# Performance work log

Measured on AMD Instinct MI355X. Metric: run time of the kernel, lower is better.

The kernel has to match this reference:

```python
import jax, jax.numpy as jnp
import numpy as np

NUM_HEADS = 8


def setup_inputs() -> dict:
    B, S, D, Q, SEG = 4, 4096, 512, 1, 256
    key = jax.random.key(0)
    ks = jax.random.split(key, 7)
    x = jax.random.normal(ks[0], (B, S, D), dtype=jnp.float32)
    seg_id = jnp.sort(jax.random.randint(ks[1], (B, S), 0, SEG), axis=-1)
    # ensure every row actually spans segment ids 0..SEG-1 so max()+1 == SEG
    seg_id = seg_id.at[:, 0].set(0).at[:, -1].set(SEG - 1)
    valid_mask = jnp.ones((B, S), dtype=bool)
    query_bank = jax.random.normal(ks[2], (1, 1, Q, D), dtype=jnp.float32)
    scale = 0.02
    w_q = jax.random.normal(ks[3], (D, D), dtype=jnp.float32) * scale
    w_k = jax.random.normal(ks[4], (D, D), dtype=jnp.float32) * scale
    w_v = jax.random.normal(ks[5], (D, D), dtype=jnp.float32) * scale
    w_o = jax.random.normal(ks[6], (D, D), dtype=jnp.float32) * scale
    return {"x": x, "seg_id": seg_id, "valid_mask": valid_mask, "s_seg_max": SEG,
            "query_bank": query_bank, "w_q": w_q, "w_k": w_k, "w_v": w_v, "w_o": w_o}


def reference(x, seg_id, valid_mask, s_seg_max, query_bank, w_q, w_k, w_v, w_o):
    B, S, D = x.shape
    Q = query_bank.shape[2]
    H = NUM_HEADS
    hd = D // H
    L = s_seg_max * Q  # number of pooled queries

    # expand learned query bank over batch and segments, project (Linear: x @ W.T)
    queries = jnp.broadcast_to(query_bank, (B, s_seg_max, Q, D)).reshape(B, L, D)
    q = (queries @ w_q.T).reshape(B, L, H, hd).transpose(0, 2, 1, 3)   # bhqd
    k = (x @ w_k.T).reshape(B, S, H, hd).transpose(0, 2, 1, 3)         # bhkd
    v = (x @ w_v.T).reshape(B, S, H, hd).transpose(0, 2, 1, 3)         # bhkd

    # torch SDPA boolean mask semantics: True = participate in attention
    seg_for_query = jnp.repeat(jnp.arange(s_seg_max), Q)               # [L]
    attend = (seg_id[:, None, :] != seg_for_query[None, :, None]) | (~valid_mask[:, None, :])  # [B,L,S]

    scores = jnp.einsum('bhqd,bhkd->bhqk', q, k) / np.sqrt(hd).astype(x.dtype)
    scores = jnp.where(attend[:, None, :, :], scores, -jnp.inf)
    attn = jax.nn.softmax(scores, axis=-1)
    out = jnp.einsum('bhqk,bhkd->bhqd', attn, v)                       # [B,H,L,hd]
    out = out.transpose(0, 2, 1, 3).reshape(B, L, D)
    return out @ w_o.T
```

## Files before the change

kernel.cpp:

```cpp
#include <hip/hip_runtime.h>
#include <hip/hip_bf16.h>


#define S 4096
#define D 512
#define H 8
#define SEG 256
#define NROW 1024

typedef short bf16x8 __attribute__((ext_vector_type(8)));
typedef float fvec4  __attribute__((ext_vector_type(4)));

constexpr int OFF_SEGO   = 0;
constexpr int OFF_DSEG   = 1032;
constexpr int OFF_NALL   = 9224;
constexpr int OFF_C16    = 11272;
constexpr int OFF_PSEG_F = 15368;
constexpr int OFF_NSEG_F = 2112520;
constexpr size_t WS_FLOATS = 2374664;

static __device__ inline ushort f2bf(float f) {
    __hip_bfloat16 h = __float2bfloat16(f);
    return *reinterpret_cast<ushort*>(&h);
}
static __device__ inline float bf2f(ushort u) {
    return __uint_as_float(((uint)u) << 16);
}
static __device__ inline uint pack2(float a, float b) {
    return (uint)f2bf(a) | ((uint)f2bf(b) << 16);
}

__global__ __launch_bounds__(512) void k_setup(const float* __restrict__ qb,
        const float* __restrict__ w_q, const float* __restrict__ w_k,
        const int* __restrict__ seg_id, float* __restrict__ W) {
    int tid = threadIdx.x, blk = blockIdx.x;
    if (blk < 8) {
        __shared__ float qbs[D];
        __shared__ float part[64][9];
        __shared__ float qp[64];
        int h = blk;
        qbs[tid] = qb[tid];
        __syncthreads();
        int jj = tid >> 3, p = tid & 7;
        const float* wr = w_q + (size_t)(h*64 + jj)*D;
        float a = 0.f;
        for (int t = 0; t < 64; ++t) a += qbs[p + 8*t] * wr[p + 8*t];
        part[jj][p] = a;
        __syncthreads();
        if (tid < 64) {
            float s = 0.f;
            #pragma unroll
            for (int p2 = 0; p2 < 8; ++p2) s += part[tid][p2];
            qp[tid] = s;
        }
        __syncthreads();
        float c = 0.f;
        for (int j2 = 0; j2 < 64; ++j2)
            c += qp[j2] * w_k[(size_t)(h*64 + j2)*D + tid];
        ((ushort*)(W + OFF_C16))[h*512 + tid] = f2bf(c * 0.125f);
    } else if (blk < 12) {
        int b = blk - 8;
        if (tid <= SEG) {
            const int* sid = seg_id + (size_t)b*S;
            int lo = 0, hi = S;
            while (lo < hi) { int mid = (lo+hi) >> 1; if (sid[mid] < tid) lo = mid+1; else hi = mid; }
            ((int*)(W + OFF_SEGO))[b*(SEG+1) + tid] = lo;
        }
    } else {
        for (int t = tid; t < 4*D; t += 512) W[OFF_NALL + t] = 0.f;
        uint* c16u = (uint*)(W + OFF_C16);
        #pragma unroll
        for (int j = 0; j < 4; ++j) c16u[2048 + tid*4 + j] = 0u;
    }
}

__global__ __launch_bounds__(256) void k_pseg(const float* __restrict__ x,
                                              float* __restrict__ W) {
    __shared__ ushort xs[32][520];
    __shared__ ushort cls[16][520];
    __shared__ float E_lds[32][12];
    int row = blockIdx.x, b = row >> 8, l = row & 255, tid = threadIdx.x;
    const ushort* c16g = (const ushort*)(W + OFF_C16);
    #pragma unroll
    for (int rep = 0; rep < 4; ++rep) {
        int q = rep*256 + tid, r = q >> 6, c8 = q & 63;
        *(bf16x8*)&cls[r][c8*8] = *(const bf16x8*)&c16g[r*512 + c8*8];
    }
    const int* off = (const int*)(W + OFF_SEGO);
    int k0 = off[b*(SEG+1) + l], k1 = off[b*(SEG+1) + l + 1];
    float2 acc[8]; float es[8];
    #pragma unroll
    for (int h = 0; h < 8; ++h) { acc[h] = make_float2(0.f,0.f); es[h] = 0.f; }
    int lane = tid & 63, wave = tid >> 6;

    for (int kc = k0; kc < k1; kc += 32) {
        int nk = min(32, k1 - kc);
        __syncthreads();
        #pragma unroll
        for (int rep = 0; rep < 16; ++rep) {
            int t4 = rep*256 + tid, r = t4 >> 7, c4 = t4 & 127;
            if (r < nk) {
                float4 v = ((const float4*)(x + (size_t)(b*S + kc + r)*D))[c4];
                uint2 u; u.x = pack2(v.x, v.y); u.y = pack2(v.z, v.w);
                *(uint2*)&xs[r][c4*4] = u;
            }
        }
        __syncthreads();
        if (wave < 2 && wave*16 < nk) {
            int m = lane & 15, kg = lane >> 4;
            fvec4 sc = {0,0,0,0};
            for (int ks = 0; ks < 512; ks += 32) {
                bf16x8 a  = *(const bf16x8*)&xs[wave*16 + m][ks + kg*8];
                bf16x8 bb = *(const bf16x8*)&cls[m][ks + kg*8];
                sc = __builtin_amdgcn_mfma_f32_16x16x32_bf16(a, bb, sc, 0, 0, 0);
            }
            int h = m;
            #pragma unroll
            for (int r = 0; r < 4; ++r) {
                int kl = wave*16 + kg*4 + r;
                if (h < 8 && kl < nk) E_lds[kl][h] = __expf(sc[r]);
            }
        }
        __syncthreads();
        for (int kk = 0; kk < nk; ++kk) {
            uint xv = *(const uint*)&xs[kk][2*tid];
            float x0 = bf2f((ushort)(xv & 0xffff));
            float x1 = bf2f((ushort)(xv >> 16));
            float4 ea = *(const float4*)&E_lds[kk][0];
            float4 eb = *(const float4*)&E_lds[kk][4];
            float e[8] = {ea.x,ea.y,ea.z,ea.w,eb.x,eb.y,eb.z,eb.w};
            #pragma unroll
            for (int h = 0; h < 8; ++h) {
                acc[h].x += e[h]*x0;
                acc[h].y += e[h]*x1;
                es[h]    += e[h];
            }
        }
    }
    uint* Pb = (uint*)(W + OFF_PSEG_F);
    #pragma unroll
    for (int h = 0; h < 8; ++h)
        Pb[(size_t)row*2048 + h*256 + tid] = pack2(acc[h].x, acc[h].y);
    if (tid == 0) {
        #pragma unroll
        for (int h = 0; h < 8; ++h) W[OFF_DSEG + row*8 + h] = es[h];
    }
}

__global__ __launch_bounds__(256) void k_gemm_v(const float* __restrict__ w_v,
                                                float* __restrict__ W) {
    __shared__ ushort As[32][520];
    __shared__ ushort Bs[64][520];
    __shared__ float colsum[2][64];
    int rt = blockIdx.x, h = blockIdx.y, tid = threadIdx.x;
    const ushort* Pb = (const ushort*)(W + OFF_PSEG_F);
    #pragma unroll
    for (int rep = 0; rep < 8; ++rep) {
        int idx = rep*256 + tid, r = idx >> 6, j = idx & 63;
        *(bf16x8*)&As[r][j*8] =
            *(const bf16x8*)&Pb[(size_t)((rt*32 + r)*8 + h)*512 + j*8];
    }
    #pragma unroll
    for (int rep = 0; rep < 32; ++rep) {
        int idx = rep*256 + tid, r = idx >> 7, c4 = idx & 127;
        float4 v = ((const float4*)(w_v + (size_t)(h*64 + r)*512))[c4];
        uint2 u; u.x = pack2(v.x, v.y); u.y = pack2(v.z, v.w);
        *(uint2*)&Bs[r][c4*4] = u;
    }
    __syncthreads();
    int lane = tid & 63, w = tid >> 6;
    int wm = w & 1, wn = w >> 1;
    int m = lane & 15, kg = lane >> 4;
    fvec4 acc0 = {0,0,0,0}, acc1 = {0,0,0,0};
    for (int ks = 0; ks < 512; ks += 32) {
        bf16x8 a  = *(const bf16x8*)&As[wm*16 + m][ks + kg*8];
        bf16x8 b0 = *(const bf16x8*)&Bs[wn*32 + m][ks + kg*8];
        bf16x8 b1 = *(const bf16x8*)&Bs[wn*32 + 16 + m][ks + kg*8];
        acc0 = __builtin_amdgcn_mfma_f32_16x16x32_bf16(a, b0, acc0, 0, 0, 0);
        acc1 = __builtin_amdgcn_mfma_f32_16x16x32_bf16(a, b1, acc1, 0, 0, 0);
    }
    ushort* NSb = (ushort*)(W + OFF_NSEG_F);
    int rowbase = rt*32 + wm*16 + kg*4;
    int col0 = h*64 + wn*32 + m, col1 = col0 + 16;
    float s0 = 0.f, s1 = 0.f;
    #pragma unroll
    for (int r = 0; r < 4; ++r) {
        NSb[(size_t)(rowbase + r)*512 + col0] = f2bf(acc0[r]);
        NSb[(size_t)(rowbase + r)*512 + col1] = f2bf(acc1[r]);
        s0 += acc0[r]; s1 += acc1[r];
    }
    s0 += __shfl_xor(s0, 16); s0 += __shfl_xor(s0, 32);
    s1 += __shfl_xor(s1, 16); s1 += __shfl_xor(s1, 32);
    if (lane < 16) {
        colsum[wm][wn*32 + lane]      = s0;
        colsum[wm][wn*32 + 16 + lane] = s1;
    }
    __syncthreads();
    if (tid < 64) {
        int b = rt >> 3;
        atomicAdd(&W[OFF_NALL + b*512 + h*64 + tid], colsum[0][tid] + colsum[1][tid]);
    }
}

__global__ __launch_bounds__(256) void k_gemm_o(const float* __restrict__ w_o,
                                                float* __restrict__ W,
                                                float* __restrict__ out) {
    __shared__ ushort As[32][520];
    __shared__ ushort Bs[64][520];
    __shared__ float NAl[512];
    __shared__ float dpart[8][8];
    __shared__ float invs[32][8];
    int rt = blockIdx.x, nt = blockIdx.y, tid = threadIdx.x;
    int b = rt >> 3;
    if (tid < 64) {
        int h = tid >> 3, sg = tid & 7;
        float s = 0.f;
        for (int l2 = sg*32; l2 < sg*32 + 32; ++l2)
            s += W[OFF_DSEG + (b*256 + l2)*8 + h];
        dpart[h][sg] = s;
    }
    NAl[tid]       = W[OFF_NALL + b*512 + tid];
    NAl[tid + 256] = W[OFF_NALL + b*512 + tid + 256];
    __syncthreads();
    {
        int r = tid >> 3, h = tid & 7;
        float da = 0.f;
        #pragma unroll
        for (int sg = 0; sg < 8; ++sg) da += dpart[h][sg];
        invs[r][h] = 1.f / (da - W[OFF_DSEG + (rt*32 + r)*8 + h]);
    }
    #pragma unroll
    for (int rep = 0; rep < 32; ++rep) {
        int idx = rep*256 + tid, r = idx >> 7, c4 = idx & 127;
        float4 v = ((const float4*)(w_o + (size_t)(nt*64 + r)*512))[c4];
        uint2 u; u.x = pack2(v.x, v.y); u.y = pack2(v.z, v.w);
        *(uint2*)&Bs[r][c4*4] = u;
    }
    __syncthreads();
    const ushort* NSb = (const ushort*)(W + OFF_NSEG_F);
    #pragma unroll
    for (int rep = 0; rep < 8; ++rep) {
        int idx = rep*256 + tid, r = idx >> 6, j = idx & 63;
        bf16x8 ns = *(const bf16x8*)&NSb[(size_t)(rt*32 + r)*512 + j*8];
        float inv = invs[r][j >> 3];
        ushort o[8];
        #pragma unroll
        for (int e = 0; e < 8; ++e)
            o[e] = f2bf((NAl[j*8 + e] - bf2f((ushort)ns[e])) * inv);
        uint4 u;
        u.x = o[0] | ((uint)o[1] << 16);
        u.y = o[2] | ((uint)o[3] << 16);
        u.z = o[4] | ((uint)o[5] << 16);
        u.w = o[6] | ((uint)o[7] << 16);
        *(uint4*)&As[r][j*8] = u;
    }
    __syncthreads();
    int lane = tid & 63, w = tid >> 6;
    int wm = w & 1, wn = w >> 1;
    int m = lane & 15, kg = lane >> 4;
    fvec4 acc0 = {0,0,0,0}, acc1 = {0,0,0,0};
    for (int ks = 0; ks < 512; ks += 32) {
        bf16x8 a  = *(const bf16x8*)&As[wm*16 + m][ks + kg*8];
        bf16x8 b0 = *(const bf16x8*)&Bs[wn*32 + m][ks + kg*8];
        bf16x8 b1 = *(const bf16x8*)&Bs[wn*32 + 16 + m][ks + kg*8];
        acc0 = __builtin_amdgcn_mfma_f32_16x16x32_bf16(a, b0, acc0, 0, 0, 0);
        acc1 = __builtin_amdgcn_mfma_f32_16x16x32_bf16(a, b1, acc1, 0, 0, 0);
    }
    int rowb = rt*32 + wm*16 + kg*4;
    int col0 = nt*64 + wn*32 + m, col1 = col0 + 16;
    #pragma unroll
    for (int r = 0; r < 4; ++r) {
        out[(size_t)(rowb + r)*512 + col0] = acc0[r];
        out[(size_t)(rowb + r)*512 + col1] = acc1[r];
    }
}

extern "C" void kernel_launch(void* const* d_in, const int* in_sizes, int n_in,
                              void* d_out, int out_size, void* d_ws, size_t ws_size,
                              hipStream_t stream) {
    const float* x   = (const float*)d_in[0];
    const int*   seg = (const int*)d_in[1];
    const float* qb  = (const float*)d_in[4];
    const float* w_q = (const float*)d_in[5];
    const float* w_k = (const float*)d_in[6];
    const float* w_v = (const float*)d_in[7];
    const float* w_o = (const float*)d_in[8];
    float* W   = (float*)d_ws;
    float* out = (float*)d_out;

    if (ws_size < WS_FLOATS * sizeof(float)) return;

    hipLaunchKernelGGL(k_setup,  dim3(13),    dim3(512), 0, stream, qb, w_q, w_k, seg, W);
    hipLaunchKernelGGL(k_pseg,   dim3(NROW),  dim3(256), 0, stream, x, W);
    hipLaunchKernelGGL(k_gemm_v, dim3(32, 8), dim3(256), 0, stream, w_v, W);
    hipLaunchKernelGGL(k_gemm_o, dim3(32, 8), dim3(256), 0, stream, w_o, W, out);
}
```

Measured before the change: 37.60 us.

## Fuse pseg, V-GEMM and O-GEMM into one launch with flag-based dataflow sync

Merges the three post-setup kernels into a single 1536-block launch. Downstream blocks spin on per-row flags and per-batch counters in workspace instead of waiting at kernel boundaries, so GEMM work can overlap with the tail of the segment-pooling phase and two launch gaps go away. The GEMM stages now stream K in 128-wide chunks through smaller shared tiles, which lowers LDS use per block. The spin-waits depend on producer blocks being scheduled before their consumers and have a timeout fallback, which risks reading stale data or burning cycles while polling.

```diff
diff --git a/kernel.cpp b/kernel.cpp
--- a/kernel.cpp
+++ b/kernel.cpp
@@ -6,7 +6,6 @@
 #define D 512
 #define H 8
 #define SEG 256
-#define NROW 1024
 
 typedef short bf16x8 __attribute__((ext_vector_type(8)));
 typedef float fvec4  __attribute__((ext_vector_type(4)));
@@ -17,7 +16,9 @@
 constexpr int OFF_C16    = 11272;
 constexpr int OFF_PSEG_F = 15368;
 constexpr int OFF_NSEG_F = 2112520;
-constexpr size_t WS_FLOATS = 2374664;
+constexpr int OFF_FLAGS  = 2374664;
+constexpr int OFF_VCNT   = 2375688;
+constexpr size_t WS_FLOATS = 2375696;
 
 static __device__ inline ushort f2bf(float f) {
     __hip_bfloat16 h = __float2bfloat16(f);
@@ -71,207 +72,250 @@
         uint* c16u = (uint*)(W + OFF_C16);
         #pragma unroll
         for (int j = 0; j < 4; ++j) c16u[2048 + tid*4 + j] = 0u;
+        uint* fl = (uint*)(W + OFF_FLAGS);
+        for (int t = tid; t < 1028; t += 512) fl[t] = 0u;
     }
 }
 
-__global__ __launch_bounds__(256) void k_pseg(const float* __restrict__ x,
-                                              float* __restrict__ W) {
-    __shared__ ushort xs[32][520];
-    __shared__ ushort cls[16][520];
-    __shared__ float E_lds[32][12];
-    int row = blockIdx.x, b = row >> 8, l = row & 255, tid = threadIdx.x;
-    const ushort* c16g = (const ushort*)(W + OFF_C16);
-    #pragma unroll
-    for (int rep = 0; rep < 4; ++rep) {
-        int q = rep*256 + tid, r = q >> 6, c8 = q & 63;
-        *(bf16x8*)&cls[r][c8*8] = *(const bf16x8*)&c16g[r*512 + c8*8];
-    }
-    const int* off = (const int*)(W + OFF_SEGO);
-    int k0 = off[b*(SEG+1) + l], k1 = off[b*(SEG+1) + l + 1];
-    float2 acc[8]; float es[8];
-    #pragma unroll
-    for (int h = 0; h < 8; ++h) { acc[h] = make_float2(0.f,0.f); es[h] = 0.f; }
+__global__ __launch_bounds__(256) void k_fused(const float* __restrict__ x,
+        const float* __restrict__ w_v, const float* __restrict__ w_o,
+        float* __restrict__ W, float* __restrict__ out) {
+    __shared__ __align__(16) char sm[51456];
+    int tid = threadIdx.x, blk = blockIdx.x;
     int lane = tid & 63, wave = tid >> 6;
-
-    for (int kc = k0; kc < k1; kc += 32) {
-        int nk = min(32, k1 - kc);
-        __syncthreads();
-        #pragma unroll
-        for (int rep = 0; rep < 16; ++rep) {
-            int t4 = rep*256 + tid, r = t4 >> 7, c4 = t4 & 127;
-            if (r < nk) {
-                float4 v = ((const float4*)(x + (size_t)(b*S + kc + r)*D))[c4];
-                uint2 u; u.x = pack2(v.x, v.y); u.y = pack2(v.z, v.w);
-                *(uint2*)&xs[r][c4*4] = u;
-            }
-        }
-        __syncthreads();
-        if (wave < 2 && wave*16 < nk) {
-            int m = lane & 15, kg = lane >> 4;
-            fvec4 sc = {0,0,0,0};
-            for (int ks = 0; ks < 512; ks += 32) {
-                bf16x8 a  = *(const bf16x8*)&xs[wave*16 + m][ks + kg*8];
-                bf16x8 bb = *(const bf16x8*)&cls[m][ks + kg*8];
-                sc = __builtin_amdgcn_mfma_f32_16x16x32_bf16(a, bb, sc, 0, 0, 0);
-            }
-            int h = m;
-            #pragma unroll
-            for (int r = 0; r < 4; ++r) {
-                int kl = wave*16 + kg*4 + r;
-                if (h < 8 && kl < nk) E_lds[kl][h] = __expf(sc[r]);
-            }
-        }
-        __syncthreads();
-        for (int kk = 0; kk < nk; ++kk) {
-            uint xv = *(const uint*)&xs[kk][2*tid];
-            float x0 = bf2f((ushort)(xv & 0xffff));
-            float x1 = bf2f((ushort)(xv >> 16));
-            float4 ea = *(const float4*)&E_lds[kk][0];
-            float4 eb = *(const float4*)&E_lds[kk][4];
-            float e[8] = {ea.x,ea.y,ea.z,ea.w,eb.x,eb.y,eb.z,eb.w};
-            #pragma unroll
-            for (int h = 0; h < 8; ++h) {
-                acc[h].x += e[h]*x0;
-                acc[h].y += e[h]*x1;
-                es[h]    += e[h];
-            }
-        }
-    }
-    uint* Pb = (uint*)(W + OFF_PSEG_F);
-    #pragma unroll
-    for (int h = 0; h < 8; ++h)
-        Pb[(size_t)row*2048 + h*256 + tid] = pack2(acc[h].x, acc[h].y);
-    if (tid == 0) {
-        #pragma unroll
-        for (int h = 0; h < 8; ++h) W[OFF_DSEG + row*8 + h] = es[h];
-    }
-}
-
-__global__ __launch_bounds__(256) void k_gemm_v(const float* __restrict__ w_v,
-                                                float* __restrict__ W) {
-    __shared__ ushort As[32][520];
-    __shared__ ushort Bs[64][520];
-    __shared__ float colsum[2][64];
-    int rt = blockIdx.x, h = blockIdx.y, tid = threadIdx.x;
-    const ushort* Pb = (const ushort*)(W + OFF_PSEG_F);
-    #pragma unroll
-    for (int rep = 0; rep < 8; ++rep) {
-        int idx = rep*256 + tid, r = idx >> 6, j = idx & 63;
-        *(bf16x8*)&As[r][j*8] =
-            *(const bf16x8*)&Pb[(size_t)((rt*32 + r)*8 + h)*512 + j*8];
-    }
-    #pragma unroll
-    for (int rep = 0; rep < 32; ++rep) {
-        int idx = rep*256 + tid, r = idx >> 7, c4 = idx & 127;
-        float4 v = ((const float4*)(w_v + (size_t)(h*64 + r)*512))[c4];
-        uint2 u; u.x = pack2(v.x, v.y); u.y = pack2(v.z, v.w);
-        *(uint2*)&Bs[r][c4*4] = u;
-    }
-    __syncthreads();
-    int lane = tid & 63, w = tid >> 6;
-    int wm = w & 1, wn = w >> 1;
-    int m = lane & 15, kg = lane >> 4;
-    fvec4 acc0 = {0,0,0,0}, acc1 = {0,0,0,0};
-    for (int ks = 0; ks < 512; ks += 32) {
-        bf16x8 a  = *(const bf16x8*)&As[wm*16 + m][ks + kg*8];
-        bf16x8 b0 = *(const bf16x8*)&Bs[wn*32 + m][ks + kg*8];
-        bf16x8 b1 = *(const bf16x8*)&Bs[wn*32 + 16 + m][ks + kg*8];
-        acc0 = __builtin_amdgcn_mfma_f32_16x16x32_bf16(a, b0, acc0, 0, 0, 0);
-        acc1 = __builtin_amdgcn_mfma_f32_16x16x32_bf16(a, b1, acc1, 0, 0, 0);
-    }
-    ushort* NSb = (ushort*)(W + OFF_NSEG_F);
-    int rowbase = rt*32 + wm*16 + kg*4;
-    int col0 = h*64 + wn*32 + m, col1 = col0 + 16;
-    float s0 = 0.f, s1 = 0.f;
-    #pragma unroll
-    for (int r = 0; r < 4; ++r) {
-        NSb[(size_t)(rowbase + r)*512 + col0] = f2bf(acc0[r]);
-        NSb[(size_t)(rowbase + r)*512 + col1] = f2bf(acc1[r]);
-        s0 += acc0[r]; s1 += acc1[r];
-    }
-    s0 += __shfl_xor(s0, 16); s0 += __shfl_xor(s0, 32);
-    s1 += __shfl_xor(s1, 16); s1 += __shfl_xor(s1, 32);
-    if (lane < 16) {
-        colsum[wm][wn*32 + lane]      = s0;
-        colsum[wm][wn*32 + 16 + lane] = s1;
-    }
-    __syncthreads();
-    if (tid < 64) {
-        int b = rt >> 3;
-        atomicAdd(&W[OFF_NALL + b*512 + h*64 + tid], colsum[0][tid] + colsum[1][tid]);
-    }
-}
-
-__global__ __launch_bounds__(256) void k_gemm_o(const float* __restrict__ w_o,
-                                                float* __restrict__ W,
-                                                float* __restrict__ out) {
-    __shared__ ushort As[32][520];
-    __shared__ ushort Bs[64][520];
-    __shared__ float NAl[512];
-    __shared__ float dpart[8][8];
-    __shared__ float invs[32][8];
-    int rt = blockIdx.x, nt = blockIdx.y, tid = threadIdx.x;
-    int b = rt >> 3;
-    if (tid < 64) {
-        int h = tid >> 3, sg = tid & 7;
-        float s = 0.f;
-        for (int l2 = sg*32; l2 < sg*32 + 32; ++l2)
-            s += W[OFF_DSEG + (b*256 + l2)*8 + h];
-        dpart[h][sg] = s;
-    }
-    NAl[tid]       = W[OFF_NALL + b*512 + tid];
-    NAl[tid + 256] = W[OFF_NALL + b*512 + tid + 256];
-    __syncthreads();
-    {
-        int r = tid >> 3, h = tid & 7;
-        float da = 0.f;
-        #pragma unroll
-        for (int sg = 0; sg < 8; ++sg) da += dpart[h][sg];
-        invs[r][h] = 1.f / (da - W[OFF_DSEG + (rt*32 + r)*8 + h]);
-    }
-    #pragma unroll
-    for (int rep = 0; rep < 32; ++rep) {
-        int idx = rep*256 + tid, r = idx >> 7, c4 = idx & 127;
-        float4 v = ((const float4*)(w_o + (size_t)(nt*64 + r)*512))[c4];
-        uint2 u; u.x = pack2(v.x, v.y); u.y = pack2(v.z, v.w);
-        *(uint2*)&Bs[r][c4*4] = u;
-    }
-    __syncthreads();
-    const ushort* NSb = (const ushort*)(W + OFF_NSEG_F);
-    #pragma unroll
-    for (int rep = 0; rep < 8; ++rep) {
-        int idx = rep*256 + tid, r = idx >> 6, j = idx & 63;
-        bf16x8 ns = *(const bf16x8*)&NSb[(size_t)(rt*32 + r)*512 + j*8];
-        float inv = invs[r][j >> 3];
-        ushort o[8];
-        #pragma unroll
-        for (int e = 0; e < 8; ++e)
-            o[e] = f2bf((NAl[j*8 + e] - bf2f((ushort)ns[e])) * inv);
-        uint4 u;
-        u.x = o[0] | ((uint)o[1] << 16);
-        u.y = o[2] | ((uint)o[3] << 16);
-        u.z = o[4] | ((uint)o[5] << 16);
-        u.w = o[6] | ((uint)o[7] << 16);
-        *(uint4*)&As[r][j*8] = u;
-    }
-    __syncthreads();
-    int lane = tid & 63, w = tid >> 6;
-    int wm = w & 1, wn = w >> 1;
-    int m = lane & 15, kg = lane >> 4;
-    fvec4 acc0 = {0,0,0,0}, acc1 = {0,0,0,0};
-    for (int ks = 0; ks < 512; ks += 32) {
-        bf16x8 a  = *(const bf16x8*)&As[wm*16 + m][ks + kg*8];
-        bf16x8 b0 = *(const bf16x8*)&Bs[wn*32 + m][ks + kg*8];
-        bf16x8 b1 = *(const bf16x8*)&Bs[wn*32 + 16 + m][ks + kg*8];
-        acc0 = __builtin_amdgcn_mfma_f32_16x16x32_bf16(a, b0, acc0, 0, 0, 0);
-        acc1 = __builtin_amdgcn_mfma_f32_16x16x32_bf16(a, b1, acc1, 0, 0, 0);
-    }
-    int rowb = rt*32 + wm*16 + kg*4;
-    int col0 = nt*64 + wn*32 + m, col1 = col0 + 16;
-    #pragma unroll
-    for (int r = 0; r < 4; ++r) {
-        out[(size_t)(rowb + r)*512 + col0] = acc0[r];
-        out[(size_t)(rowb + r)*512 + col1] = acc1[r];
+    uint* flags = (uint*)(W + OFF_FLAGS);
+    uint* vcnt  = (uint*)(W + OFF_VCNT);
+
+    if (blk < 1024) {
+        ushort* xs  = (ushort*)sm;
+        ushort* cls = (ushort*)(sm + 33280);
+        float*  E   = (float*)(sm + 49920);
+        int row = blk, b = row >> 8, l = row & 255;
+        const ushort* c16g = (const ushort*)(W + OFF_C16);
+        #pragma unroll
+        for (int rep = 0; rep < 4; ++rep) {
+            int q = rep*256 + tid, r = q >> 6, c8 = q & 63;
+            *(bf16x8*)&cls[r*520 + c8*8] = *(const bf16x8*)&c16g[r*512 + c8*8];
+        }
+        const int* off = (const int*)(W + OFF_SEGO);
+        int k0 = __builtin_amdgcn_readfirstlane(off[b*(SEG+1) + l]);
+        int k1 = __builtin_amdgcn_readfirstlane(off[b*(SEG+1) + l + 1]);
+        float2 acc[8]; float es[8];
+        #pragma unroll
+        for (int h = 0; h < 8; ++h) { acc[h] = make_float2(0.f,0.f); es[h] = 0.f; }
+        for (int kc = k0; kc < k1; kc += 32) {
+            int nk = min(32, k1 - kc);
+            __syncthreads();
+            #pragma unroll
+            for (int rep = 0; rep < 16; ++rep) {
+                int t4 = rep*256 + tid, r = t4 >> 7, c4 = t4 & 127;
+                if (r < nk) {
+                    float4 v = ((const float4*)(x + (size_t)(b*S + kc + r)*D))[c4];
+                    uint2 u; u.x = pack2(v.x, v.y); u.y = pack2(v.z, v.w);
+                    *(uint2*)&xs[r*520 + c4*4] = u;
+                }
+            }
+            __syncthreads();
+            if (wave < 2 && wave*16 < nk) {
+                int m = lane & 15, kg = lane >> 4;
+                fvec4 sc = {0,0,0,0};
+                for (int ks = 0; ks < 512; ks += 32) {
+                    bf16x8 a  = *(const bf16x8*)&xs[(wave*16 + m)*520 + ks + kg*8];
+                    bf16x8 bb = *(const bf16x8*)&cls[m*520 + ks + kg*8];
+                    sc = __builtin_amdgcn_mfma_f32_16x16x32_bf16(a, bb, sc, 0, 0, 0);
+                }
+                #pragma unroll
+                for (int r = 0; r < 4; ++r) {
+                    int kl = wave*16 + kg*4 + r;
+                    if (m < 8 && kl < nk) E[kl*12 + m] = __expf(sc[r]);
+                }
+            }
+            __syncthreads();
+            for (int kk = 0; kk < nk; ++kk) {
+                uint xv = *(const uint*)&xs[kk*520 + 2*tid];
+                float x0 = bf2f((ushort)(xv & 0xffff));
+                float x1 = bf2f((ushort)(xv >> 16));
+                float4 ea = *(const float4*)&E[kk*12];
+                float4 eb = *(const float4*)&E[kk*12 + 4];
+                float e[8] = {ea.x,ea.y,ea.z,ea.w,eb.x,eb.y,eb.z,eb.w};
+                #pragma unroll
+                for (int h = 0; h < 8; ++h) {
+                    acc[h].x += e[h]*x0;
+                    acc[h].y += e[h]*x1;
+                    es[h]    += e[h];
+                }
+            }
+        }
+        uint* Pb = (uint*)(W + OFF_PSEG_F);
+        #pragma unroll
+        for (int h = 0; h < 8; ++h)
+            Pb[(size_t)row*2048 + h*256 + tid] = pack2(acc[h].x, acc[h].y);
+        if (tid == 0) {
+            #pragma unroll
+            for (int h = 0; h < 8; ++h) W[OFF_DSEG + row*8 + h] = es[h];
+        }
+        __syncthreads();
+        if (tid == 0) {
+            __threadfence();
+            __hip_atomic_store(&flags[row], 1u, __ATOMIC_RELAXED,
+                               __HIP_MEMORY_SCOPE_AGENT);
+        }
+    } else if (blk < 1280) {
+        int id = blk - 1024, rt = id & 31, h = id >> 5, b = rt >> 3;
+        if (tid < 32) {
+            int spins = 1 << 18;
+            while (__hip_atomic_load(&flags[rt*32 + tid], __ATOMIC_RELAXED,
+                                     __HIP_MEMORY_SCOPE_AGENT) == 0u) {
+                __builtin_amdgcn_s_sleep(2);
+                if (--spins == 0) break;
+            }
+        }
+        __syncthreads();
+        __threadfence();
+        ushort* As = (ushort*)sm;
+        ushort* Bs = (ushort*)(sm + 8704);
+        float* colsum = (float*)(sm + 26112);
+        const ushort* Pb = (const ushort*)(W + OFF_PSEG_F);
+        int wm = wave & 1, wn = wave >> 1;
+        int m = lane & 15, kg = lane >> 4;
+        fvec4 acc0 = {0,0,0,0}, acc1 = {0,0,0,0};
+        for (int kc = 0; kc < 4; ++kc) {
+            __syncthreads();
+            #pragma unroll
+            for (int rep = 0; rep < 2; ++rep) {
+                int idx = rep*256 + tid, r = idx >> 4, j8 = idx & 15;
+                *(bf16x8*)&As[r*136 + j8*8] =
+                    *(const bf16x8*)&Pb[(size_t)((rt*32 + r)*8 + h)*512 + kc*128 + j8*8];
+            }
+            #pragma unroll
+            for (int rep = 0; rep < 4; ++rep) {
+                int idx = rep*256 + tid, r = idx >> 4, j8 = idx & 15;
+                const float4* s4 = (const float4*)(w_v + (size_t)(h*64 + r)*512 + kc*128 + j8*8);
+                float4 v0 = s4[0], v1 = s4[1];
+                uint4 u;
+                u.x = pack2(v0.x, v0.y); u.y = pack2(v0.z, v0.w);
+                u.z = pack2(v1.x, v1.y); u.w = pack2(v1.z, v1.w);
+                *(uint4*)&Bs[r*136 + j8*8] = u;
+            }
+            __syncthreads();
+            #pragma unroll
+            for (int ks = 0; ks < 128; ks += 32) {
+                bf16x8 a  = *(const bf16x8*)&As[(wm*16 + m)*136 + ks + kg*8];
+                bf16x8 b0 = *(const bf16x8*)&Bs[(wn*32 + m)*136 + ks + kg*8];
+                bf16x8 b1 = *(const bf16x8*)&Bs[(wn*32 + 16 + m)*136 + ks + kg*8];
+                acc0 = __builtin_amdgcn_mfma_f32_16x16x32_bf16(a, b0, acc0, 0, 0, 0);
+                acc1 = __builtin_amdgcn_mfma_f32_16x16x32_bf16(a, b1, acc1, 0, 0, 0);
+            }
+        }
+        ushort* NSb = (ushort*)(W + OFF_NSEG_F);
+        int rowbase = rt*32 + wm*16 + kg*4;
+        int col0 = h*64 + wn*32 + m, col1 = col0 + 16;
+        float s0 = 0.f, s1 = 0.f;
+        #pragma unroll
+        for (int r = 0; r < 4; ++r) {
+            NSb[(size_t)(rowbase + r)*512 + col0] = f2bf(acc0[r]);
+            NSb[(size_t)(rowbase + r)*512 + col1] = f2bf(acc1[r]);
+            s0 += acc0[r]; s1 += acc1[r];
+        }
+        s0 += __shfl_xor(s0, 16); s0 += __shfl_xor(s0, 32);
+        s1 += __shfl_xor(s1, 16); s1 += __shfl_xor(s1, 32);
+        if (lane < 16) {
+            colsum[wm*64 + wn*32 + lane]      = s0;
+            colsum[wm*64 + wn*32 + 16 + lane] = s1;
+        }
+        __syncthreads();
+        if (tid < 64)
+            atomicAdd(&W[OFF_NALL + b*512 + h*64 + tid], colsum[tid] + colsum[64 + tid]);
+        __syncthreads();
+        if (tid == 0) {
+            __threadfence();
+            __hip_atomic_fetch_add(&vcnt[b], 1u, __ATOMIC_RELAXED,
+                                   __HIP_MEMORY_SCOPE_AGENT);
+        }
+    } else {
+        int id = blk - 1280, rt = id & 31, nt = id >> 5, b = rt >> 3;
+        if (tid == 0) {
+            int spins = 1 << 18;
+            while (__hip_atomic_load(&vcnt[b], __ATOMIC_RELAXED,
+                                     __HIP_MEMORY_SCOPE_AGENT) < 64u) {
+                __builtin_amdgcn_s_sleep(2);
+                if (--spins == 0) break;
+            }
+        }
+        __syncthreads();
+        __threadfence();
+        ushort* As   = (ushort*)sm;
+        ushort* Bs   = (ushort*)(sm + 8704);
+        float* NAl   = (float*)(sm + 26112);
+        float* dpart = (float*)(sm + 28160);
+        float* invs  = (float*)(sm + 28416);
+        if (tid < 64) {
+            int h = tid >> 3, sg = tid & 7;
+            float s = 0.f;
+            for (int l2 = sg*32; l2 < sg*32 + 32; ++l2)
+                s += W[OFF_DSEG + (b*256 + l2)*8 + h];
+            dpart[h*8 + sg] = s;
+        }
+        NAl[tid]       = W[OFF_NALL + b*512 + tid];
+        NAl[tid + 256] = W[OFF_NALL + b*512 + tid + 256];
+        __syncthreads();
+        {
+            int r = tid >> 3, h = tid & 7;
+            float da = 0.f;
+            #pragma unroll
+            for (int sg = 0; sg < 8; ++sg) da += dpart[h*8 + sg];
+            invs[r*8 + h] = 1.f / (da - W[OFF_DSEG + (rt*32 + r)*8 + h]);
+        }
+        const ushort* NSb = (const ushort*)(W + OFF_NSEG_F);
+        int wm = wave & 1, wn = wave >> 1;
+        int m = lane & 15, kg = lane >> 4;
+        fvec4 acc0 = {0,0,0,0}, acc1 = {0,0,0,0};
+        for (int kc = 0; kc < 4; ++kc) {
+            __syncthreads();
+            #pragma unroll
+            for (int rep = 0; rep < 2; ++rep) {
+                int idx = rep*256 + tid, r = idx >> 4, j8 = idx & 15;
+                int jc = kc*128 + j8*8;
+                bf16x8 ns = *(const bf16x8*)&NSb[(size_t)(rt*32 + r)*512 + jc];
+                float inv = invs[r*8 + (jc >> 6)];
+                ushort o[8];
+                #pragma unroll
+                for (int e = 0; e < 8; ++e)
+                    o[e] = f2bf((NAl[jc + e] - bf2f((ushort)ns[e])) * inv);
+                uint4 u;
+                u.x = o[0] | ((uint)o[1] << 16);
+                u.y = o[2] | ((uint)o[3] << 16);
+                u.z = o[4] | ((uint)o[5] << 16);
+                u.w = o[6] | ((uint)o[7] << 16);
+                *(uint4*)&As[r*136 + j8*8] = u;
+            }
+            #pragma unroll
+            for (int rep = 0; rep < 4; ++rep) {
+                int idx = rep*256 + tid, r = idx >> 4, j8 = idx & 15;
+                const float4* s4 = (const float4*)(w_o + (size_t)(nt*64 + r)*512 + kc*128 + j8*8);
+                float4 v0 = s4[0], v1 = s4[1];
+                uint4 u;
+                u.x = pack2(v0.x, v0.y); u.y = pack2(v0.z, v0.w);
+                u.z = pack2(v1.x, v1.y); u.w = pack2(v1.z, v1.w);
+                *(uint4*)&Bs[r*136 + j8*8] = u;
+            }
+            __syncthreads();
+            #pragma unroll
+            for (int ks = 0; ks < 128; ks += 32) {
+                bf16x8 a  = *(const bf16x8*)&As[(wm*16 + m)*136 + ks + kg*8];
+                bf16x8 b0 = *(const bf16x8*)&Bs[(wn*32 + m)*136 + ks + kg*8];
+                bf16x8 b1 = *(const bf16x8*)&Bs[(wn*32 + 16 + m)*136 + ks + kg*8];
+                acc0 = __builtin_amdgcn_mfma_f32_16x16x32_bf16(a, b0, acc0, 0, 0, 0);
+                acc1 = __builtin_amdgcn_mfma_f32_16x16x32_bf16(a, b1, acc1, 0, 0, 0);
+            }
+        }
+        int rowb = rt*32 + wm*16 + kg*4;
+        int col0 = nt*64 + wn*32 + m, col1 = col0 + 16;
+        #pragma unroll
+        for (int r = 0; r < 4; ++r) {
+            out[(size_t)(rowb + r)*512 + col0] = acc0[r];
+            out[(size_t)(rowb + r)*512 + col1] = acc1[r];
+        }
     }
 }
 
@@ -290,8 +334,6 @@
 
     if (ws_size < WS_FLOATS * sizeof(float)) return;
 
-    hipLaunchKernelGGL(k_setup,  dim3(13),    dim3(512), 0, stream, qb, w_q, w_k, seg, W);
-    hipLaunchKernelGGL(k_pseg,   dim3(NROW),  dim3(256), 0, stream, x, W);
-    hipLaunchKernelGGL(k_gemm_v, dim3(32, 8), dim3(256), 0, stream, w_v, W);
-    hipLaunchKernelGGL(k_gemm_o, dim3(32, 8), dim3(256), 0, stream, w_o, W, out);
-}
+    hipLaunchKernelGGL(k_setup, dim3(13),   dim3(512), 0, stream, qb, w_q, w_k, seg, W);
+    hipLaunchKernelGGL(k_fused, dim3(1536), dim3(256), 0, stream, x, w_v, w_o, W, out);
+}
```

New measurement: 146.4 us. +289.5%, slower.

## Fold w_v and w_o into per-head combined matrix, merge GEMM kernels

Applied to the files above, without the earlier changes.

Precomputes a per-head product of w_o and w_v slices (M = Wo_h·Wv_h) inside the setup kernel, parallelised across many more blocks. The pseg kernel now atomically accumulates the full-sequence pooled sums and softmax denominators. A single output kernel then applies the segment-exclusion normalisation and multiplies by M, replacing the separate V-projection and output-projection kernels. This removes one launch and the intermediate projected-value buffer, but raises the output GEMM's reduction depth eightfold (K=4096) and adds many global atomics in pseg.

```diff
diff --git a/kernel.cpp b/kernel.cpp
--- a/kernel.cpp
+++ b/kernel.cpp
@@ -6,18 +6,18 @@
 #define D 512
 #define H 8
 #define SEG 256
-#define NROW 1024
 
 typedef short bf16x8 __attribute__((ext_vector_type(8)));
 typedef float fvec4  __attribute__((ext_vector_type(4)));
 
 constexpr int OFF_SEGO   = 0;
 constexpr int OFF_DSEG   = 1032;
-constexpr int OFF_NALL   = 9224;
-constexpr int OFF_C16    = 11272;
-constexpr int OFF_PSEG_F = 15368;
-constexpr int OFF_NSEG_F = 2112520;
-constexpr size_t WS_FLOATS = 2374664;
+constexpr int OFF_DALL   = 9224;
+constexpr int OFF_PALL   = 9256;
+constexpr int OFF_C16    = 25640;
+constexpr int OFF_PSEG_F = 29736;
+constexpr int OFF_M_F    = 2126888;
+constexpr size_t WS_FLOATS = 3175464;
 
 static __device__ inline ushort f2bf(float f) {
     __hip_bfloat16 h = __float2bfloat16(f);
@@ -30,47 +30,111 @@
     return (uint)f2bf(a) | ((uint)f2bf(b) << 16);
 }
 
-__global__ __launch_bounds__(512) void k_setup(const float* __restrict__ qb,
+__global__ __launch_bounds__(256) void k_setup(const float* __restrict__ qb,
         const float* __restrict__ w_q, const float* __restrict__ w_k,
+        const float* __restrict__ w_v, const float* __restrict__ w_o,
         const int* __restrict__ seg_id, float* __restrict__ W) {
     int tid = threadIdx.x, blk = blockIdx.x;
-    if (blk < 8) {
-        __shared__ float qbs[D];
-        __shared__ float part[64][9];
+    if (blk < 64) {
+        __shared__ float qbs[512];
+        __shared__ float red[64*5];
         __shared__ float qp[64];
-        int h = blk;
+        int h = blk >> 3, oct = blk & 7;
         qbs[tid] = qb[tid];
-        __syncthreads();
-        int jj = tid >> 3, p = tid & 7;
-        const float* wr = w_q + (size_t)(h*64 + jj)*D;
-        float a = 0.f;
-        for (int t = 0; t < 64; ++t) a += qbs[p + 8*t] * wr[p + 8*t];
-        part[jj][p] = a;
+        qbs[tid + 256] = qb[tid + 256];
+        __syncthreads();
+        {
+            int jj = tid >> 2, q = tid & 3;
+            const float4* wr = (const float4*)(w_q + (size_t)(h*64 + jj)*D + q*128);
+            const float4* qv = (const float4*)(qbs + q*128);
+            float a = 0.f;
+            #pragma unroll
+            for (int t = 0; t < 32; ++t) {
+                float4 wv = wr[t], xv = qv[t];
+                a += wv.x*xv.x + wv.y*xv.y + wv.z*xv.z + wv.w*xv.w;
+            }
+            red[jj*5 + q] = a;
+        }
+        __syncthreads();
+        if (tid < 64)
+            qp[tid] = red[tid*5] + red[tid*5+1] + red[tid*5+2] + red[tid*5+3];
+        __syncthreads();
+        {
+            int il = tid >> 2, jq = tid & 3;
+            int i = oct*64 + il;
+            float c = 0.f;
+            #pragma unroll
+            for (int j = 0; j < 16; ++j)
+                c += qp[jq*16 + j] * w_k[(size_t)(h*64 + jq*16 + j)*D + i];
+            red[il*5 + jq] = c;
+        }
         __syncthreads();
         if (tid < 64) {
-            float s = 0.f;
-            #pragma unroll
-            for (int p2 = 0; p2 < 8; ++p2) s += part[tid][p2];
-            qp[tid] = s;
-        }
-        __syncthreads();
-        float c = 0.f;
-        for (int j2 = 0; j2 < 64; ++j2)
-            c += qp[j2] * w_k[(size_t)(h*64 + j2)*D + tid];
-        ((ushort*)(W + OFF_C16))[h*512 + tid] = f2bf(c * 0.125f);
-    } else if (blk < 12) {
-        int b = blk - 8;
-        if (tid <= SEG) {
-            const int* sid = seg_id + (size_t)b*S;
-            int lo = 0, hi = S;
-            while (lo < hi) { int mid = (lo+hi) >> 1; if (sid[mid] < tid) lo = mid+1; else hi = mid; }
-            ((int*)(W + OFF_SEGO))[b*(SEG+1) + tid] = lo;
-        }
+            float cc = red[tid*5] + red[tid*5+1] + red[tid*5+2] + red[tid*5+3];
+            ((ushort*)(W + OFF_C16))[h*512 + oct*64 + tid] = f2bf(cc * 0.125f);
+        }
+    } else if (blk < 68) {
+        int b = blk - 64;
+        const int* sid = seg_id + (size_t)b*S;
+        int* offp = (int*)(W + OFF_SEGO);
+        int lo = 0, hi = S;
+        while (lo < hi) { int mid = (lo+hi) >> 1; if (sid[mid] < tid) lo = mid+1; else hi = mid; }
+        offp[b*257 + tid] = lo;
+        if (tid == 0) offp[b*257 + 256] = S;
+    } else if (blk == 68) {
+        for (int t = tid; t < 16416; t += 256) W[OFF_DALL + t] = 0.f;
+        uint* c16u = (uint*)(W + OFF_C16);
+        #pragma unroll
+        for (int j = 0; j < 8; ++j) c16u[2048 + tid*8 + j] = 0u;
     } else {
-        for (int t = tid; t < 4*D; t += 512) W[OFF_NALL + t] = 0.f;
-        uint* c16u = (uint*)(W + OFF_C16);
-        #pragma unroll
-        for (int j = 0; j < 4; ++j) c16u[2048 + tid*4 + j] = 0u;
+        __shared__ __align__(16) ushort As[32][72];
+        __shared__ __align__(16) ushort Bs[64][72];
+        int id = blk - 69;
+        int h = id >> 7, rem = id & 127, jt = rem >> 3, dt = rem & 7;
+        {
+            int r = tid >> 3, c8 = tid & 7;
+            const float4* s4 = (const float4*)(w_o + (size_t)(jt*32 + r)*D + h*64 + c8*8);
+            float4 v0 = s4[0], v1 = s4[1];
+            uint4 u;
+            u.x = pack2(v0.x, v0.y); u.y = pack2(v0.z, v0.w);
+            u.z = pack2(v1.x, v1.y); u.w = pack2(v1.z, v1.w);
+            *(uint4*)&As[r][c8*8] = u;
+        }
+        {
+            int i = tid >> 2, dg = tid & 3;
+            const float4* s4 = (const float4*)(w_v + (size_t)(h*64 + i)*D + dt*64 + dg*16);
+            float4 v0 = s4[0], v1 = s4[1], v2 = s4[2], v3 = s4[3];
+            float vv[16] = {v0.x,v0.y,v0.z,v0.w, v1.x,v1.y,v1.z,v1.w,
+                            v2.x,v2.y,v2.z,v2.w, v3.x,v3.y,v3.z,v3.w};
+            #pragma unroll
+            for (int q = 0; q < 16; ++q) Bs[dg*16 + q][i] = f2bf(vv[q]);
+        }
+        __syncthreads();
+        int lane = tid & 63, wave = tid >> 6;
+        int wm = wave & 1, wn = wave >> 1;
+        int m = lane & 15, kg = lane >> 4;
+        fvec4 acc = {0,0,0,0};
+        #pragma unroll
+        for (int ks = 0; ks < 64; ks += 32) {
+            bf16x8 a  = *(const bf16x8*)&As[wm*16 + m][ks + kg*8];
+            bf16x8 b0 = *(const bf16x8*)&Bs[wn*32 + m][ks + kg*8];
+            acc = __builtin_amdgcn_mfma_f32_16x16x32_bf16(a, b0, acc, 0, 0, 0);
+        }
+        fvec4 acc1 = {0,0,0,0};
+        #pragma unroll
+        for (int ks = 0; ks < 64; ks += 32) {
+            bf16x8 a  = *(const bf16x8*)&As[wm*16 + m][ks + kg*8];
+            bf16x8 b1 = *(const bf16x8*)&Bs[wn*32 + 16 + m][ks + kg*8];
+            acc1 = __builtin_amdgcn_mfma_f32_16x16x32_bf16(a, b1, acc1, 0, 0, 0);
+        }
+        ushort* Mb = (ushort*)(W + OFF_M_F);
+        int jrow = jt*32 + wm*16 + kg*4;
+        int col0 = dt*64 + wn*32 + m, col1 = col0 + 16;
+        #pragma unroll
+        for (int r = 0; r < 4; ++r) {
+            Mb[(size_t)(h*512 + jrow + r)*512 + col0] = f2bf(acc[r]);
+            Mb[(size_t)(h*512 + jrow + r)*512 + col1] = f2bf(acc1[r]);
+        }
     }
 }
 
@@ -87,12 +151,12 @@
         *(bf16x8*)&cls[r][c8*8] = *(const bf16x8*)&c16g[r*512 + c8*8];
     }
     const int* off = (const int*)(W + OFF_SEGO);
-    int k0 = off[b*(SEG+1) + l], k1 = off[b*(SEG+1) + l + 1];
+    int k0 = __builtin_amdgcn_readfirstlane(off[b*(SEG+1) + l]);
+    int k1 = __builtin_amdgcn_readfirstlane(off[b*(SEG+1) + l + 1]);
     float2 acc[8]; float es[8];
     #pragma unroll
     for (int h = 0; h < 8; ++h) { acc[h] = make_float2(0.f,0.f); es[h] = 0.f; }
     int lane = tid & 63, wave = tid >> 6;
-
     for (int kc = k0; kc < k1; kc += 32) {
         int nk = min(32, k1 - kc);
         __syncthreads();
@@ -114,11 +178,10 @@
                 bf16x8 bb = *(const bf16x8*)&cls[m][ks + kg*8];
                 sc = __builtin_amdgcn_mfma_f32_16x16x32_bf16(a, bb, sc, 0, 0, 0);
             }
-            int h = m;
             #pragma unroll
             for (int r = 0; r < 4; ++r) {
                 int kl = wave*16 + kg*4 + r;
-                if (h < 8 && kl < nk) E_lds[kl][h] = __expf(sc[r]);
+                if (m < 8 && kl < nk) E_lds[kl][m] = __expf(sc[r]);
             }
         }
         __syncthreads();
@@ -139,132 +202,76 @@
     }
     uint* Pb = (uint*)(W + OFF_PSEG_F);
     #pragma unroll
-    for (int h = 0; h < 8; ++h)
+    for (int h = 0; h < 8; ++h) {
         Pb[(size_t)row*2048 + h*256 + tid] = pack2(acc[h].x, acc[h].y);
+        atomicAdd(&W[OFF_PALL + b*4096 + h*512 + 2*tid],     acc[h].x);
+        atomicAdd(&W[OFF_PALL + b*4096 + h*512 + 2*tid + 1], acc[h].y);
+    }
     if (tid == 0) {
         #pragma unroll
-        for (int h = 0; h < 8; ++h) W[OFF_DSEG + row*8 + h] = es[h];
-    }
-}
-
-__global__ __launch_bounds__(256) void k_gemm_v(const float* __restrict__ w_v,
-                                                float* __restrict__ W) {
-    __shared__ ushort As[32][520];
-    __shared__ ushort Bs[64][520];
-    __shared__ float colsum[2][64];
-    int rt = blockIdx.x, h = blockIdx.y, tid = threadIdx.x;
-    const ushort* Pb = (const ushort*)(W + OFF_PSEG_F);
-    #pragma unroll
-    for (int rep = 0; rep < 8; ++rep) {
-        int idx = rep*256 + tid, r = idx >> 6, j = idx & 63;
-        *(bf16x8*)&As[r][j*8] =
-            *(const bf16x8*)&Pb[(size_t)((rt*32 + r)*8 + h)*512 + j*8];
-    }
-    #pragma unroll
-    for (int rep = 0; rep < 32; ++rep) {
-        int idx = rep*256 + tid, r = idx >> 7, c4 = idx & 127;
-        float4 v = ((const float4*)(w_v + (size_t)(h*64 + r)*512))[c4];
-        uint2 u; u.x = pack2(v.x, v.y); u.y = pack2(v.z, v.w);
-        *(uint2*)&Bs[r][c4*4] = u;
-    }
-    __syncthreads();
-    int lane = tid & 63, w = tid >> 6;
-    int wm = w & 1, wn = w >> 1;
-    int m = lane & 15, kg = lane >> 4;
-    fvec4 acc0 = {0,0,0,0}, acc1 = {0,0,0,0};
-    for (int ks = 0; ks < 512; ks += 32) {
-        bf16x8 a  = *(const bf16x8*)&As[wm*16 + m][ks + kg*8];
-        bf16x8 b0 = *(const bf16x8*)&Bs[wn*32 + m][ks + kg*8];
-        bf16x8 b1 = *(const bf16x8*)&Bs[wn*32 + 16 + m][ks + kg*8];
-        acc0 = __builtin_amdgcn_mfma_f32_16x16x32_bf16(a, b0, acc0, 0, 0, 0);
-        acc1 = __builtin_amdgcn_mfma_f32_16x16x32_bf16(a, b1, acc1, 0, 0, 0);
-    }
-    ushort* NSb = (ushort*)(W + OFF_NSEG_F);
-    int rowbase = rt*32 + wm*16 + kg*4;
-    int col0 = h*64 + wn*32 + m, col1 = col0 + 16;
-    float s0 = 0.f, s1 = 0.f;
-    #pragma unroll
-    for (int r = 0; r < 4; ++r) {
-        NSb[(size_t)(rowbase + r)*512 + col0] = f2bf(acc0[r]);
-        NSb[(size_t)(rowbase + r)*512 + col1] = f2bf(acc1[r]);
-        s0 += acc0[r]; s1 += acc1[r];
-    }
-    s0 += __shfl_xor(s0, 16); s0 += __shfl_xor(s0, 32);
-    s1 += __shfl_xor(s1, 16); s1 += __shfl_xor(s1, 32);
-    if (lane < 16) {
-        colsum[wm][wn*32 + lane]      = s0;
-        colsum[wm][wn*32 + 16 + lane] = s1;
-    }
-    __syncthreads();
-    if (tid < 64) {
-        int b = rt >> 3;
-        atomicAdd(&W[OFF_NALL + b*512 + h*64 + tid], colsum[0][tid] + colsum[1][tid]);
-    }
-}
-
-__global__ __launch_bounds__(256) void k_gemm_o(const float* __restrict__ w_o,
-                                                float* __restrict__ W,
-                                                float* __restrict__ out) {
-    __shared__ ushort As[32][520];
-    __shared__ ushort Bs[64][520];
-    __shared__ float NAl[512];
-    __shared__ float dpart[8][8];
+        for (int h = 0; h < 8; ++h) {
+            W[OFF_DSEG + row*8 + h] = es[h];
+            atomicAdd(&W[OFF_DALL + b*8 + h], es[h]);
+        }
+    }
+}
+
+__global__ __launch_bounds__(256) void k_out(float* __restrict__ W,
+                                             float* __restrict__ out) {
+    __shared__ __align__(16) ushort As[32][136];
+    __shared__ __align__(16) ushort Bs[64][136];
+    __shared__ float PAl[4096];
     __shared__ float invs[32][8];
     int rt = blockIdx.x, nt = blockIdx.y, tid = threadIdx.x;
     int b = rt >> 3;
-    if (tid < 64) {
-        int h = tid >> 3, sg = tid & 7;
-        float s = 0.f;
-        for (int l2 = sg*32; l2 < sg*32 + 32; ++l2)
-            s += W[OFF_DSEG + (b*256 + l2)*8 + h];
-        dpart[h][sg] = s;
-    }
-    NAl[tid]       = W[OFF_NALL + b*512 + tid];
-    NAl[tid + 256] = W[OFF_NALL + b*512 + tid + 256];
-    __syncthreads();
+    for (int i = tid; i < 4096; i += 256) PAl[i] = W[OFF_PALL + b*4096 + i];
     {
         int r = tid >> 3, h = tid & 7;
-        float da = 0.f;
-        #pragma unroll
-        for (int sg = 0; sg < 8; ++sg) da += dpart[h][sg];
-        invs[r][h] = 1.f / (da - W[OFF_DSEG + (rt*32 + r)*8 + h]);
-    }
-    #pragma unroll
-    for (int rep = 0; rep < 32; ++rep) {
-        int idx = rep*256 + tid, r = idx >> 7, c4 = idx & 127;
-        float4 v = ((const float4*)(w_o + (size_t)(nt*64 + r)*512))[c4];
-        uint2 u; u.x = pack2(v.x, v.y); u.y = pack2(v.z, v.w);
-        *(uint2*)&Bs[r][c4*4] = u;
+        invs[r][h] = 1.f / (W[OFF_DALL + b*8 + h] - W[OFF_DSEG + (rt*32 + r)*8 + h]);
     }
     __syncthreads();
-    const ushort* NSb = (const ushort*)(W + OFF_NSEG_F);
-    #pragma unroll
-    for (int rep = 0; rep < 8; ++rep) {
-        int idx = rep*256 + tid, r = idx >> 6, j = idx & 63;
-        bf16x8 ns = *(const bf16x8*)&NSb[(size_t)(rt*32 + r)*512 + j*8];
-        float inv = invs[r][j >> 3];
-        ushort o[8];
-        #pragma unroll
-        for (int e = 0; e < 8; ++e)
-            o[e] = f2bf((NAl[j*8 + e] - bf2f((ushort)ns[e])) * inv);
-        uint4 u;
-        u.x = o[0] | ((uint)o[1] << 16);
-        u.y = o[2] | ((uint)o[3] << 16);
-        u.z = o[4] | ((uint)o[5] << 16);
-        u.w = o[6] | ((uint)o[7] << 16);
-        *(uint4*)&As[r][j*8] = u;
-    }
-    __syncthreads();
-    int lane = tid & 63, w = tid >> 6;
-    int wm = w & 1, wn = w >> 1;
+    const ushort* Pb = (const ushort*)(W + OFF_PSEG_F);
+    const ushort* Mb = (const ushort*)(W + OFF_M_F);
+    int lane = tid & 63, wave = tid >> 6;
+    int wm = wave & 1, wn = wave >> 1;
     int m = lane & 15, kg = lane >> 4;
     fvec4 acc0 = {0,0,0,0}, acc1 = {0,0,0,0};
-    for (int ks = 0; ks < 512; ks += 32) {
-        bf16x8 a  = *(const bf16x8*)&As[wm*16 + m][ks + kg*8];
-        bf16x8 b0 = *(const bf16x8*)&Bs[wn*32 + m][ks + kg*8];
-        bf16x8 b1 = *(const bf16x8*)&Bs[wn*32 + 16 + m][ks + kg*8];
-        acc0 = __builtin_amdgcn_mfma_f32_16x16x32_bf16(a, b0, acc0, 0, 0, 0);
-        acc1 = __builtin_amdgcn_mfma_f32_16x16x32_bf16(a, b1, acc1, 0, 0, 0);
+    for (int h = 0; h < 8; ++h) {
+        for (int kc = 0; kc < 4; ++kc) {
+            __syncthreads();
+            #pragma unroll
+            for (int rep = 0; rep < 2; ++rep) {
+                int idx = rep*256 + tid, r = idx >> 4, j8 = idx & 15;
+                bf16x8 ps = *(const bf16x8*)&Pb[(size_t)((rt*32 + r)*8 + h)*512 + kc*128 + j8*8];
+                float inv = invs[r][h];
+                const float* pa = &PAl[h*512 + kc*128 + j8*8];
+                ushort q[8];
+                #pragma unroll
+                for (int e = 0; e < 8; ++e)
+                    q[e] = f2bf((pa[e] - bf2f((ushort)ps[e])) * inv);
+                uint4 u;
+                u.x = q[0] | ((uint)q[1] << 16);
+                u.y = q[2] | ((uint)q[3] << 16);
+                u.z = q[4] | ((uint)q[5] << 16);
+                u.w = q[6] | ((uint)q[7] << 16);
+                *(uint4*)&As[r][j8*8] = u;
+            }
+            #pragma unroll
+            for (int rep = 0; rep < 4; ++rep) {
+                int idx = rep*256 + tid, r = idx >> 4, j8 = idx & 15;
+                *(bf16x8*)&Bs[r][j8*8] =
+                    *(const bf16x8*)&Mb[(size_t)(h*512 + nt*64 + r)*512 + kc*128 + j8*8];
+            }
+            __syncthreads();
+            #pragma unroll
+            for (int ks = 0; ks < 128; ks += 32) {
+                bf16x8 a  = *(const bf16x8*)&As[wm*16 + m][ks + kg*8];
+                bf16x8 b0 = *(const bf16x8*)&Bs[wn*32 + m][ks + kg*8];
+                bf16x8 b1 = *(const bf16x8*)&Bs[wn*32 + 16 + m][ks + kg*8];
+                acc0 = __builtin_amdgcn_mfma_f32_16x16x32_bf16(a, b0, acc0, 0, 0, 0);
+                acc1 = __builtin_amdgcn_mfma_f32_16x16x32_bf16(a, b1, acc1, 0, 0, 0);
+            }
+        }
     }
     int rowb = rt*32 + wm*16 + kg*4;
     int col0 = nt*64 + wn*32 + m, col1 = col0 + 16;
@@ -290,8 +297,8 @@
 
     if (ws_size < WS_FLOATS * sizeof(float)) return;
 
-    hipLaunchKernelGGL(k_setup,  dim3(13),    dim3(512), 0, stream, qb, w_q, w_k, seg, W);
-    hipLaunchKernelGGL(k_pseg,   dim3(NROW),  dim3(256), 0, stream, x, W);
-    hipLaunchKernelGGL(k_gemm_v, dim3(32, 8), dim3(256), 0, stream, w_v, W);
-    hipLaunchKernelGGL(k_gemm_o, dim3(32, 8), dim3(256), 0, stream, w_o, W, out);
-}
+    hipLaunchKernelGGL(k_setup, dim3(1093),  dim3(256), 0, stream,
+                       qb, w_q, w_k, w_v, w_o, seg, W);
+    hipLaunchKernelGGL(k_pseg,  dim3(1024),  dim3(256), 0, stream, x, W);
+    hipLaunchKernelGGL(k_out,   dim3(32, 8), dim3(256), 0, stream, W, out);
+}
```

Result: slower. 143.5 us (+281.7%).
